# Optimization experiments

Hardware: AMD Instinct MI355X
Metric: run time of the kernel (lower is better)

The kernel has to match this reference:

```python
import jax, jax.numpy as jnp
import numpy as np

B, C, H, W = 4, 256, 64, 64
CQK = C // 8


def setup_inputs() -> dict:
    key = jax.random.key(0)
    ks = jax.random.split(key, 7)
    s = 1.0 / np.sqrt(C)
    return {
        "x": jax.random.normal(ks[0], (B, C, H, W), dtype=jnp.float32),
        "Wq": jax.random.normal(ks[1], (CQK, C), dtype=jnp.float32) * s,
        "bq": jax.random.normal(ks[2], (CQK,), dtype=jnp.float32) * 0.01,
        "Wk": jax.random.normal(ks[3], (CQK, C), dtype=jnp.float32) * s,
        "bk": jax.random.normal(ks[4], (CQK,), dtype=jnp.float32) * 0.01,
        "Wv": jax.random.normal(ks[5], (C, C), dtype=jnp.float32) * s,
        "bv": jax.random.normal(ks[6], (C,), dtype=jnp.float32) * 0.01,
    }


def reference(x, Wq, bq, Wk, bk, Wv, bv):
    b, c, h, w = x.shape
    n = h * w
    xf = x.reshape(b, c, n)                                   # [B,C,N]
    # 1x1 convs == per-pixel channel projections
    q = jnp.einsum('oc,bcn->bon', Wq, xf) + bq[None, :, None]  # [B,C/8,N]
    k = jnp.einsum('oc,bcn->bon', Wk, xf) + bk[None, :, None]  # [B,C/8,N]
    v = jnp.einsum('oc,bcn->bon', Wv, xf) + bv[None, :, None]  # [B,C,N]
    # energy[b,i,j] = <q[:, i], k[:, j]>  (no scaling, as in the original)
    energy = jnp.einsum('boi,boj->bij', q, k)                  # [B,N,N]
    attn = jax.nn.softmax(energy, axis=-1)                     # [B,N,N]
    # out[b,c,i] = sum_j v[b,c,j] * attn[b,i,j]
    out = jnp.einsum('bcj,bij->bci', v, attn)                  # [B,C,N]
    return out.reshape(b, c, h, w) + x
```

## Files before the change

kernel.cpp:

```cpp
#include <hip/hip_runtime.h>
#include <hip/hip_bf16.h>
#include <math.h>

#define B_DIM 4
#define C_DIM 256
#define CQK_DIM 32
#define N_POS 4096
#define NPART 4

typedef unsigned short u16;
typedef __attribute__((ext_vector_type(8))) short bf16x8;
typedef __attribute__((ext_vector_type(4))) float f32x4;

__device__ __forceinline__ u16 f32_to_bf16_rn(float f) {
    union { float f; unsigned int u; } v; v.f = f;
    unsigned int u = v.u;
    u += 0x7fffu + ((u >> 16) & 1u);
    return (u16)(u >> 16);
}
__device__ __forceinline__ float bf16_to_f32(u16 h) {
    union { unsigned int u; float f; } v; v.u = ((unsigned int)h) << 16;
    return v.f;
}
__device__ __forceinline__ void async_copy16(const u16* g, u16* l) {
    __builtin_amdgcn_global_load_lds(
        (const __attribute__((address_space(1))) void*)g,
        (__attribute__((address_space(3))) void*)l, 16, 0, 0);
}


__global__ __launch_bounds__(256) void proj_kernel(
    const float* __restrict__ x,
    const float* __restrict__ Wq, const float* __restrict__ bq,
    const float* __restrict__ Wk, const float* __restrict__ bk,
    const float* __restrict__ Wv, const float* __restrict__ bv,
    u16* __restrict__ qhi, u16* __restrict__ qlo,
    u16* __restrict__ kth, u16* __restrict__ ktl,
    u16* __restrict__ vtile)
{
    const int t    = threadIdx.x;
    const int blk  = blockIdx.x;
    const int b    = blk >> 6;
    const int jt   = blk & 63;
    const int n0   = jt * 64;
    const int wave = t >> 6;
    const int lane = t & 63;
    const int n16  = lane & 15;
    const int quad = lane >> 4;
    const float* xb = x + (size_t)b * C_DIM * N_POS;

    f32x4 accV[4][4];
    f32x4 accQ[4];
    #pragma unroll
    for (int v = 0; v < 4; ++v)
        #pragma unroll
        for (int nt = 0; nt < 4; ++nt) accV[v][nt] = (f32x4){0.f,0.f,0.f,0.f};
    #pragma unroll
    for (int nt = 0; nt < 4; ++nt) accQ[nt] = (f32x4){0.f,0.f,0.f,0.f};

    const float* Wqk  = (wave < 2) ? Wq : Wk;
    const int    qkrow = (wave & 1) * 16 + n16;

    for (int kk = 0; kk < 8; ++kk) {
        const int k0 = kk * 32 + quad * 8;
        bf16x8 bh[4], bl[4];
        #pragma unroll
        for (int nt = 0; nt < 4; ++nt) {
            const float* xp = xb + (size_t)k0 * N_POS + n0 + nt * 16 + n16;
            float xv[8];
            #pragma unroll
            for (int j = 0; j < 8; ++j) xv[j] = xp[(size_t)j * N_POS];
            #pragma unroll
            for (int j = 0; j < 8; ++j) {
                u16 h = f32_to_bf16_rn(xv[j]);
                bh[nt][j] = (short)h;
                bl[nt][j] = (short)f32_to_bf16_rn(xv[j] - bf16_to_f32(h));
            }
        }
        #pragma unroll
        for (int v = 0; v < 4; ++v) {
            const float* wr = Wv + (size_t)(wave * 64 + v * 16 + n16) * C_DIM + k0;
            float4 a0 = *(const float4*)(wr);
            float4 a1 = *(const float4*)(wr + 4);
            bf16x8 ah;
            ah[0] = (short)f32_to_bf16_rn(a0.x); ah[1] = (short)f32_to_bf16_rn(a0.y);
            ah[2] = (short)f32_to_bf16_rn(a0.z); ah[3] = (short)f32_to_bf16_rn(a0.w);
            ah[4] = (short)f32_to_bf16_rn(a1.x); ah[5] = (short)f32_to_bf16_rn(a1.y);
            ah[6] = (short)f32_to_bf16_rn(a1.z); ah[7] = (short)f32_to_bf16_rn(a1.w);
            #pragma unroll
            for (int nt = 0; nt < 4; ++nt)
                accV[v][nt] = __builtin_amdgcn_mfma_f32_16x16x32_bf16(
                    ah, bh[nt], accV[v][nt], 0, 0, 0);
        }
        {
            const float* wr = Wqk + (size_t)qkrow * C_DIM + k0;
            bf16x8 ah, al;
            #pragma unroll
            for (int j = 0; j < 8; ++j) {
                float w = wr[j];
                u16 h = f32_to_bf16_rn(w);
                ah[j] = (short)h;
                al[j] = (short)f32_to_bf16_rn(w - bf16_to_f32(h));
            }
            #pragma unroll
            for (int nt = 0; nt < 4; ++nt) {
                accQ[nt] = __builtin_amdgcn_mfma_f32_16x16x32_bf16(ah, bh[nt], accQ[nt], 0, 0, 0);
                accQ[nt] = __builtin_amdgcn_mfma_f32_16x16x32_bf16(ah, bl[nt], accQ[nt], 0, 0, 0);
                accQ[nt] = __builtin_amdgcn_mfma_f32_16x16x32_bf16(al, bh[nt], accQ[nt], 0, 0, 0);
            }
        }
    }

    u16* vt = vtile + (size_t)(b * 64 + jt) * (32 * 512);
    #pragma unroll
    for (int v = 0; v < 4; ++v) {
        const int cb = wave * 4 + v;
        #pragma unroll
        for (int r = 0; r < 4; ++r) {
            const int c = cb * 16 + quad * 4 + r;
            const float bias = bv[c];
            #pragma unroll
            for (int nt = 0; nt < 4; ++nt) {
                const int kb = nt >> 1;
                const int qd = (nt & 1) * 2 + (n16 >> 3);
                vt[(cb * 2 + kb) * 512 + (qd * 16 + quad * 4 + r) * 8 + (n16 & 7)] =
                    f32_to_bf16_rn(accV[v][nt][r] + bias);
            }
        }
    }
    if (wave < 2) {
        #pragma unroll
        for (int r = 0; r < 4; ++r) {
            const int c = (wave & 1) * 16 + quad * 4 + r;
            const float bias = bq[c];
            #pragma unroll
            for (int nt = 0; nt < 4; ++nt) {
                float val = accQ[nt][r] + bias;
                u16 h = f32_to_bf16_rn(val);
                u16 lo = f32_to_bf16_rn(val - bf16_to_f32(h));
                size_t base = ((size_t)b * N_POS + n0 + nt * 16 + n16) * CQK_DIM + c;
                qhi[base] = h; qlo[base] = lo;
            }
        }
    } else {
        u16* kh_t = kth + (size_t)(b * 64 + jt) * (4 * 512);
        u16* kl_t = ktl + (size_t)(b * 64 + jt) * (4 * 512);
        #pragma unroll
        for (int r = 0; r < 4; ++r) {
            const int c = (wave & 1) * 16 + quad * 4 + r;
            const float bias = bk[c];
            #pragma unroll
            for (int nt = 0; nt < 4; ++nt) {
                float val = accQ[nt][r] + bias;
                u16 h = f32_to_bf16_rn(val);
                u16 lo = f32_to_bf16_rn(val - bf16_to_f32(h));
                const int off = nt * 512 + ((c >> 3) * 16 + n16) * 8 + (c & 7);
                kh_t[off] = h; kl_t[off] = lo;
            }
        }
    }
}

__global__ __launch_bounds__(256, 2) void flash_kernel(
    const u16* __restrict__ qhi, const u16* __restrict__ qlo,
    const u16* __restrict__ kth, const u16* __restrict__ ktl,
    const u16* __restrict__ vtile,
    u16* __restrict__ part, float2* __restrict__ ml)
{
    __shared__ u16 Vt[2][32 * 512];
    __shared__ u16 pbuf[4][2 * 512];

    const int t    = threadIdx.x;
    const int wave = t >> 6;
    const int lane = t & 63;
    const int n16  = lane & 15;
    const int quad = lane >> 4;

    const int idx    = blockIdx.x;
    const int xcd    = idx & 7;
    const int b      = xcd & 3;
    const int z      = idx >> 3;
    const int p      = z & 3;
    const int iouter = z >> 2;
    const int itile  = (iouter << 1) | (xcd >> 2);
    const int i0     = itile * 128 + wave * 32;

    bf16x8 qh[2], ql[2];
    #pragma unroll
    for (int m = 0; m < 2; ++m) {
        qh[m] = *(const bf16x8*)(qhi + ((size_t)b * N_POS + i0 + m * 16 + n16) * CQK_DIM + quad * 8);
        ql[m] = *(const bf16x8*)(qlo + ((size_t)b * N_POS + i0 + m * 16 + n16) * CQK_DIM + quad * 8);
    }

    f32x4 O[2][16];
    #pragma unroll
    for (int m = 0; m < 2; ++m)
        #pragma unroll
        for (int cb = 0; cb < 16; ++cb) O[m][cb] = (f32x4){0.f, 0.f, 0.f, 0.f};
    float lsum[2][4] = {{0.f,0.f,0.f,0.f},{0.f,0.f,0.f,0.f}};

    u16* pb = pbuf[wave];
    const int jt_beg = p * 16;
    const int jt_end = jt_beg + 16;

    {
        const u16* vsrc = vtile + (size_t)(b * 64 + jt_beg) * (32 * 512);
        for (int ch = wave; ch < 32; ch += 4)
            async_copy16(vsrc + ch * 512 + lane * 8, Vt[0] + ch * 512);
    }

    int buf = 0;
    for (int jt = jt_beg; jt < jt_end; ++jt) {
        const u16* kh_t = kth + (size_t)(b * 64 + jt) * (4 * 512);
        const u16* kl_t = ktl + (size_t)(b * 64 + jt) * (4 * 512);
        bf16x8 kh[4], kl[4];
        #pragma unroll
        for (int jb = 0; jb < 4; ++jb) {
            kh[jb] = *(const bf16x8*)(kh_t + jb * 512 + lane * 8);
            kl[jb] = *(const bf16x8*)(kl_t + jb * 512 + lane * 8);
        }
        __syncthreads();

        if (jt + 1 < jt_end) {
            const u16* vsrc = vtile + (size_t)(b * 64 + jt + 1) * (32 * 512);
            for (int ch = wave; ch < 32; ch += 4)
                async_copy16(vsrc + ch * 512 + lane * 8, Vt[buf ^ 1] + ch * 512);
        }

        f32x4 s[2][4];
        #pragma unroll
        for (int m = 0; m < 2; ++m)
            #pragma unroll
            for (int jb = 0; jb < 4; ++jb) {
                f32x4 acc = (f32x4){0.f, 0.f, 0.f, 0.f};
                acc = __builtin_amdgcn_mfma_f32_16x16x32_bf16(qh[m], kh[jb], acc, 0, 0, 0);
                acc = __builtin_amdgcn_mfma_f32_16x16x32_bf16(qh[m], kl[jb], acc, 0, 0, 0);
                acc = __builtin_amdgcn_mfma_f32_16x16x32_bf16(ql[m], kh[jb], acc, 0, 0, 0);
                s[m][jb] = acc;
            }
        #pragma unroll
        for (int m = 0; m < 2; ++m)
            #pragma unroll
            for (int jb = 0; jb < 4; ++jb)
                #pragma unroll
                for (int r = 0; r < 4; ++r) {
                    float pv = __expf(s[m][jb][r]);
                    s[m][jb][r] = pv;
                    lsum[m][r] += pv;
                }

        const u16* vb = Vt[buf];
        #pragma unroll
        for (int kb = 0; kb < 2; ++kb) {
            #pragma unroll
            for (int m = 0; m < 2; ++m)
                #pragma unroll
                for (int j2 = 0; j2 < 2; ++j2) {
                    const int jb = kb * 2 + j2;
                    const int fr = m * 512 +
                        ((j2 * 2 + (n16 >> 3)) * 16 + quad * 4) * 8 + (n16 & 7);
                    #pragma unroll
                    for (int r = 0; r < 4; ++r)
                        pb[fr + r * 8] = f32_to_bf16_rn(s[m][jb][r]);
                }
            asm volatile("s_waitcnt lgkmcnt(0)" ::: "memory");
            bf16x8 Pf[2];
            #pragma unroll
            for (int m = 0; m < 2; ++m)
                Pf[m] = *(const bf16x8*)(pb + m * 512 + lane * 8);
            #pragma unroll
            for (int cb = 0; cb < 16; ++cb) {
                bf16x8 Vf = *(const bf16x8*)(vb + (cb * 2 + kb) * 512 + lane * 8);
                #pragma unroll
                for (int m = 0; m < 2; ++m)
                    O[m][cb] = __builtin_amdgcn_mfma_f32_16x16x32_bf16(
                        Pf[m], Vf, O[m][cb], 0, 0, 0);
            }
        }
        buf ^= 1;
    }

    #pragma unroll
    for (int off = 1; off <= 8; off <<= 1)
        #pragma unroll
        for (int m = 0; m < 2; ++m)
            #pragma unroll
            for (int r = 0; r < 4; ++r)
                lsum[m][r] += __shfl_xor(lsum[m][r], off, 64);
    float inv_l[2][4];
    #pragma unroll
    for (int m = 0; m < 2; ++m)
        #pragma unroll
        for (int r = 0; r < 4; ++r) inv_l[m][r] = 1.f / lsum[m][r];

    u16* pbase = part + ((size_t)(p * 4 + b) * N_POS + i0) * C_DIM;
    #pragma unroll
    for (int m = 0; m < 2; ++m)
        #pragma unroll
        for (int cb = 0; cb < 16; ++cb)
            #pragma unroll
            for (int r = 0; r < 4; ++r)
                pbase[(size_t)(m * 16 + quad * 4 + r) * C_DIM + cb * 16 + n16] =
                    f32_to_bf16_rn(O[m][cb][r] * inv_l[m][r]);
    if (n16 == 0) {
        #pragma unroll
        for (int m = 0; m < 2; ++m)
            #pragma unroll
            for (int r = 0; r < 4; ++r)
                ml[(size_t)(p * 4 + b) * N_POS + i0 + m * 16 + quad * 4 + r] =
                    make_float2(0.f, lsum[m][r]);
    }
}

__global__ __launch_bounds__(256) void reduce_kernel(
    const u16* __restrict__ part, const float2* __restrict__ ml,
    const float* __restrict__ x, float* __restrict__ out)
{
    const int TJ = 32;
    __shared__ float wgt[NPART][TJ];
    __shared__ float trans[C_DIM][TJ + 1];

    const int t   = threadIdx.x;
    const int blk = blockIdx.x;
    const int b   = blk >> 7;
    const int n0  = (blk & 127) * TJ;

    if (t < TJ) {
        int i = n0 + t;
        float s = 0.f, w[NPART];
        #pragma unroll
        for (int p = 0; p < NPART; ++p) {
            float2 a = ml[(size_t)(p * 4 + b) * N_POS + i];
            w[p] = a.y;
            s += w[p];
        }
        float inv = 1.f / s;
        #pragma unroll
        for (int p = 0; p < NPART; ++p) wgt[p][t] = w[p] * inv;
    }
    __syncthreads();

    {
        const int cp = t & 127;
        const int ih = t >> 7;
        for (int ib = 0; ib < TJ; ib += 2) {
            int i = ib + ih;
            float acc0 = 0.f, acc1 = 0.f;
            #pragma unroll
            for (int p = 0; p < NPART; ++p) {
                const u16* row = part + ((size_t)(p * 4 + b) * N_POS + n0 + i) * C_DIM;
                ushort2 pv = ((const ushort2*)row)[cp];
                float wp = wgt[p][i];
                acc0 += wp * bf16_to_f32(pv.x);
                acc1 += wp * bf16_to_f32(pv.y);
            }
            trans[2 * cp][i]     = acc0;
            trans[2 * cp + 1][i] = acc1;
        }
    }
    __syncthreads();

    {
        const int il = t & 31;
        const int cr = t >> 5;
        const float* xb = x + (size_t)b * C_DIM * N_POS;
        float* ob       = out + (size_t)b * C_DIM * N_POS;
        for (int cc = 0; cc < 32; ++cc) {
            int c = cc * 8 + cr;
            size_t g = (size_t)c * N_POS + n0 + il;
            ob[g] = trans[c][il] + xb[g];
        }
    }
}

extern "C" void kernel_launch(void* const* d_in, const int* in_sizes, int n_in,
                              void* d_out, int out_size, void* d_ws, size_t ws_size,
                              hipStream_t stream) {
    const float* x  = (const float*)d_in[0];
    const float* Wq = (const float*)d_in[1];
    const float* bq = (const float*)d_in[2];
    const float* Wk = (const float*)d_in[3];
    const float* bk = (const float*)d_in[4];
    const float* Wv = (const float*)d_in[5];
    const float* bv = (const float*)d_in[6];
    float* out = (float*)d_out;

    char* ws = (char*)d_ws;
    u16*    qhi   = (u16*)(ws);
    u16*    qlo   = (u16*)(ws + (1ull << 20));
    u16*    kth   = (u16*)(ws + (2ull << 20));
    u16*    ktl   = (u16*)(ws + (3ull << 20));
    u16*    vtile = (u16*)(ws + (4ull << 20));
    u16*    part  = (u16*)(ws + (12ull << 20));
    float2* mlp   = (float2*)(ws + (44ull << 20));

    hipLaunchKernelGGL(proj_kernel, dim3(256), dim3(256), 0, stream,
                       x, Wq, bq, Wk, bk, Wv, bv, qhi, qlo, kth, ktl, vtile);
    hipLaunchKernelGGL(flash_kernel, dim3(512), dim3(256), 0, stream,
                       qhi, qlo, kth, ktl, vtile, part, mlp);
    hipLaunchKernelGGL(reduce_kernel, dim3(512), dim3(256), 0, stream,
                       part, mlp, x, out);
}
```

Measured before the change: 89.09 us.

## Compute transposed QK scores so P stays in registers for PV MFMA

Swaps the MFMA operand order in the score computation so each lane holds a row of scores in the layout the PV MFMA A-operand expects. This removes the per-tile LDS round-trip for P (stores, waitcnt, reloads) and the pbuf shared allocation. The V tile layout in the projection kernel is permuted to match the new key ordering, and row sums now use a cross-quad shuffle plus a broadcast. It also adds s_setprio around the MFMA sections to favour matrix issue across waves.

Result: slower. 91.48 us (+2.7%).

```diff
diff --git a/kernel.cpp b/kernel.cpp
--- a/kernel.cpp
+++ b/kernel.cpp
@@ -122,8 +122,9 @@
             #pragma unroll
             for (int nt = 0; nt < 4; ++nt) {
                 const int kb = nt >> 1;
-                const int qd = (nt & 1) * 2 + (n16 >> 3);
-                vt[(cb * 2 + kb) * 512 + (qd * 16 + quad * 4 + r) * 8 + (n16 & 7)] =
+                vt[(cb * 2 + kb) * 512
+                   + ((n16 >> 2) * 16 + quad * 4 + r) * 8
+                   + (nt & 1) * 4 + (n16 & 3)] =
                     f32_to_bf16_rn(accV[v][nt][r] + bias);
             }
         }
@@ -168,7 +169,6 @@
     u16* __restrict__ part, float2* __restrict__ ml)
 {
     __shared__ u16 Vt[2][32 * 512];
-    __shared__ u16 pbuf[4][2 * 512];
 
     const int t    = threadIdx.x;
     const int wave = t >> 6;
@@ -197,9 +197,8 @@
     for (int m = 0; m < 2; ++m)
         #pragma unroll
         for (int cb = 0; cb < 16; ++cb) O[m][cb] = (f32x4){0.f, 0.f, 0.f, 0.f};
-    float lsum[2][4] = {{0.f,0.f,0.f,0.f},{0.f,0.f,0.f,0.f}};
-
-    u16* pb = pbuf[wave];
+    float lsum[2] = {0.f, 0.f};
+
     const int jt_beg = p * 16;
     const int jt_end = jt_beg + 16;
 
@@ -228,16 +227,20 @@
         }
 
         f32x4 s[2][4];
+        __builtin_amdgcn_s_setprio(1);
         #pragma unroll
         for (int m = 0; m < 2; ++m)
             #pragma unroll
             for (int jb = 0; jb < 4; ++jb) {
                 f32x4 acc = (f32x4){0.f, 0.f, 0.f, 0.f};
-                acc = __builtin_amdgcn_mfma_f32_16x16x32_bf16(qh[m], kh[jb], acc, 0, 0, 0);
-                acc = __builtin_amdgcn_mfma_f32_16x16x32_bf16(qh[m], kl[jb], acc, 0, 0, 0);
-                acc = __builtin_amdgcn_mfma_f32_16x16x32_bf16(ql[m], kh[jb], acc, 0, 0, 0);
+                acc = __builtin_amdgcn_mfma_f32_16x16x32_bf16(kh[jb], qh[m], acc, 0, 0, 0);
+                acc = __builtin_amdgcn_mfma_f32_16x16x32_bf16(kl[jb], qh[m], acc, 0, 0, 0);
+                acc = __builtin_amdgcn_mfma_f32_16x16x32_bf16(kh[jb], ql[m], acc, 0, 0, 0);
                 s[m][jb] = acc;
             }
+        __builtin_amdgcn_s_setprio(0);
+
+        bf16x8 Pf[2][2];
         #pragma unroll
         for (int m = 0; m < 2; ++m)
             #pragma unroll
@@ -245,53 +248,38 @@
                 #pragma unroll
                 for (int r = 0; r < 4; ++r) {
                     float pv = __expf(s[m][jb][r]);
-                    s[m][jb][r] = pv;
-                    lsum[m][r] += pv;
+                    lsum[m] += pv;
+                    Pf[m][jb >> 1][(jb & 1) * 4 + r] = (short)f32_to_bf16_rn(pv);
                 }
 
         const u16* vb = Vt[buf];
+        __builtin_amdgcn_s_setprio(1);
         #pragma unroll
         for (int kb = 0; kb < 2; ++kb) {
-            #pragma unroll
-            for (int m = 0; m < 2; ++m)
-                #pragma unroll
-                for (int j2 = 0; j2 < 2; ++j2) {
-                    const int jb = kb * 2 + j2;
-                    const int fr = m * 512 +
-                        ((j2 * 2 + (n16 >> 3)) * 16 + quad * 4) * 8 + (n16 & 7);
-                    #pragma unroll
-                    for (int r = 0; r < 4; ++r)
-                        pb[fr + r * 8] = f32_to_bf16_rn(s[m][jb][r]);
-                }
-            asm volatile("s_waitcnt lgkmcnt(0)" ::: "memory");
-            bf16x8 Pf[2];
-            #pragma unroll
-            for (int m = 0; m < 2; ++m)
-                Pf[m] = *(const bf16x8*)(pb + m * 512 + lane * 8);
             #pragma unroll
             for (int cb = 0; cb < 16; ++cb) {
                 bf16x8 Vf = *(const bf16x8*)(vb + (cb * 2 + kb) * 512 + lane * 8);
                 #pragma unroll
                 for (int m = 0; m < 2; ++m)
                     O[m][cb] = __builtin_amdgcn_mfma_f32_16x16x32_bf16(
-                        Pf[m], Vf, O[m][cb], 0, 0, 0);
-            }
-        }
+                        Pf[m][kb], Vf, O[m][cb], 0, 0, 0);
+            }
+        }
+        __builtin_amdgcn_s_setprio(0);
         buf ^= 1;
     }
 
     #pragma unroll
-    for (int off = 1; off <= 8; off <<= 1)
-        #pragma unroll
-        for (int m = 0; m < 2; ++m)
-            #pragma unroll
-            for (int r = 0; r < 4; ++r)
-                lsum[m][r] += __shfl_xor(lsum[m][r], off, 64);
+    for (int m = 0; m < 2; ++m) {
+        lsum[m] += __shfl_xor(lsum[m], 16, 64);
+        lsum[m] += __shfl_xor(lsum[m], 32, 64);
+    }
     float inv_l[2][4];
     #pragma unroll
     for (int m = 0; m < 2; ++m)
         #pragma unroll
-        for (int r = 0; r < 4; ++r) inv_l[m][r] = 1.f / lsum[m][r];
+        for (int r = 0; r < 4; ++r)
+            inv_l[m][r] = 1.f / __shfl(lsum[m], quad * 4 + r, 64);
 
     u16* pbase = part + ((size_t)(p * 4 + b) * N_POS + i0) * C_DIM;
     #pragma unroll
@@ -302,13 +290,11 @@
             for (int r = 0; r < 4; ++r)
                 pbase[(size_t)(m * 16 + quad * 4 + r) * C_DIM + cb * 16 + n16] =
                     f32_to_bf16_rn(O[m][cb][r] * inv_l[m][r]);
-    if (n16 == 0) {
+    if (quad == 0) {
         #pragma unroll
         for (int m = 0; m < 2; ++m)
-            #pragma unroll
-            for (int r = 0; r < 4; ++r)
-                ml[(size_t)(p * 4 + b) * N_POS + i0 + m * 16 + quad * 4 + r] =
-                    make_float2(0.f, lsum[m][r]);
+            ml[(size_t)(p * 4 + b) * N_POS + i0 + m * 16 + n16] =
+                make_float2(0.f, lsum[m]);
     }
 }
 
```
